# Kernel optimization log

Hardware: AMD Instinct MI355X
Metric: run time of the kernel (lower is better)

Reference implementation:

```python
import jax, jax.numpy as jnp
import numpy as np

N_NODES = 100000
N_EDGES = 3200000
IN_DIM = 128
HIDDEN = 128
N_GRAPHS = 64


def setup_inputs() -> dict:
    key = jax.random.key(0)
    ks = jax.random.split(key, 16)
    feat = jax.random.normal(ks[0], (N_NODES, IN_DIM), dtype=jnp.float32)
    src = jax.random.randint(ks[1], (N_EDGES,), 0, N_NODES, dtype=jnp.int32)
    dst = jax.random.randint(ks[2], (N_EDGES,), 0, N_NODES, dtype=jnp.int32)
    graph_ids = jnp.sort(jax.random.randint(ks[3], (N_NODES,), 0, N_GRAPHS, dtype=jnp.int32))
    # GraphConv weights (in_feats, out_feats) + bias, DGL default glorot-ish scale
    def lin(k, fi, fo):
        s = 1.0 / np.sqrt(fi)
        kw, kb = jax.random.split(k)
        W = jax.random.uniform(kw, (fi, fo), jnp.float32, -s, s)
        b = jax.random.uniform(kb, (fo,), jnp.float32, -s, s)
        return W, b
    W1, b1 = lin(ks[4], IN_DIM, HIDDEN)
    W2, b2 = lin(ks[5], HIDDEN, HIDDEN)
    # MLPReadout(128, 1, L=3): 128->64->32->16->1
    Wm0, bm0 = lin(ks[6], 128, 64)
    Wm1, bm1 = lin(ks[7], 64, 32)
    Wm2, bm2 = lin(ks[8], 32, 16)
    Wm3, bm3 = lin(ks[9], 16, 1)
    return dict(feat=feat, src=src, dst=dst, graph_ids=graph_ids, num_graphs=N_GRAPHS,
                W1=W1, b1=b1, W2=W2, b2=b2,
                Wm0=Wm0, bm0=bm0, Wm1=Wm1, bm1=bm1, Wm2=Wm2, bm2=bm2, Wm3=Wm3, bm3=bm3)


def reference(feat, src, dst, graph_ids, num_graphs,
              W1, b1, W2, b2,
              Wm0, bm0, Wm1, bm1, Wm2, bm2, Wm3, bm3):
    N = feat.shape[0]
    ones_e = jnp.ones(src.shape[0], dtype=feat.dtype)
    # DGL GraphConv norm='both': D_out^{-1/2} on src side, D_in^{-1/2} on dst side,
    # degrees clamped to >=1 (allow_zero_in_degree=True)
    deg_out = jnp.clip(jax.ops.segment_sum(ones_e, src, num_segments=N), 1.0)
    deg_in = jnp.clip(jax.ops.segment_sum(ones_e, dst, num_segments=N), 1.0)
    norm_src = jax.lax.rsqrt(deg_out)[:, None]  # [N,1]
    norm_dst = jax.lax.rsqrt(deg_in)[:, None]

    def gconv(h, W, b):
        h = h * norm_src
        agg = jax.ops.segment_sum(h[src], dst, num_segments=N)  # SpMM: [N,d]
        return agg * norm_dst @ W + b

    h = jax.nn.relu(gconv(feat, W1, b1))
    h = jax.nn.relu(gconv(h, W2, b2))

    # dgl.mean_nodes: per-graph mean over nodes
    counts = jnp.clip(jax.ops.segment_sum(jnp.ones(N, dtype=h.dtype), graph_ids, num_segments=num_graphs), 1.0)
    hg = jax.ops.segment_sum(h, graph_ids, num_segments=num_graphs) / counts[:, None]  # [G, hidden]

    # MLPReadout
    y = jax.nn.relu(hg @ Wm0 + bm0)
    y = jax.nn.relu(y @ Wm1 + bm1)
    y = jax.nn.relu(y @ Wm2 + bm2)
    return y @ Wm3 + bm3  # [G, 1]
```

## Files before the change

kernel.cpp:

```cpp
#include <hip/hip_runtime.h>
#include <hip/hip_fp16.h>

#define N_NODES 100000
#define N_EDGES 3200000
#define DIM 128
#define NG 64
#define GS_CHUNKS 16

#define KSH 9
#define BKT 512
#define NBKT ((N_NODES + BKT - 1) / BKT)
#define CHUNK 16384
#define NBLK ((N_EDGES + CHUNK - 1) / CHUNK)

using f16x8 = __attribute__((ext_vector_type(8))) _Float16;
using f32x4 = __attribute__((ext_vector_type(4))) float;

__global__ __launch_bounds__(256) void k_hist1(const int* __restrict__ src, const int* __restrict__ dst,
                                               int* __restrict__ histD, int* __restrict__ histS) {
    __shared__ int hD[NBKT];
    __shared__ int hS[NBKT];
    int t = threadIdx.x, blk = blockIdx.x;
    for (int i = t; i < NBKT; i += 256) { hD[i] = 0; hS[i] = 0; }
    __syncthreads();
    int base = blk * CHUNK;
    for (int i = t; i < CHUNK; i += 256) {
        int e = base + i;
        if (e < N_EDGES) {
            atomicAdd(&hD[dst[e] >> KSH], 1);
            atomicAdd(&hS[src[e] >> KSH], 1);
        }
    }
    __syncthreads();
    for (int i = t; i < NBKT; i += 256) {
        histD[i * NBLK + blk] = hD[i];
        histS[i * NBLK + blk] = hS[i];
    }
}

__global__ __launch_bounds__(256) void k_rowsum(const int* __restrict__ histD,
                                                const int* __restrict__ histS,
                                                int* __restrict__ rowtot) {
    __shared__ int red[256];
    int r = blockIdx.x;
    const int* a = (r < NBKT) ? (histD + (size_t)r * NBLK) : (histS + (size_t)(r - NBKT) * NBLK);
    int t = threadIdx.x;
    int s = 0;
    for (int i = t; i < NBLK; i += 256) s += a[i];
    red[t] = s;
    __syncthreads();
    for (int off = 128; off > 0; off >>= 1) {
        if (t < off) red[t] += red[t + off];
        __syncthreads();
    }
    if (t == 0) rowtot[r] = red[0];
}

__global__ void k_basescan(int* __restrict__ rowtot) {
    __shared__ int sh[256];
    int t = threadIdx.x;
    int o0 = (t < NBKT) ? rowtot[t] : 0;
    int o1 = (t < NBKT) ? rowtot[NBKT + t] : 0;
    sh[t] = o0; __syncthreads();
    for (int off = 1; off < 256; off <<= 1) {
        int v = sh[t]; int u = (t >= off) ? sh[t - off] : 0;
        __syncthreads(); sh[t] = v + u; __syncthreads();
    }
    int e0 = sh[t] - o0;
    __syncthreads();
    sh[t] = o1; __syncthreads();
    for (int off = 1; off < 256; off <<= 1) {
        int v = sh[t]; int u = (t >= off) ? sh[t - off] : 0;
        __syncthreads(); sh[t] = v + u; __syncthreads();
    }
    int e1 = sh[t] - o1;
    if (t < NBKT) { rowtot[t] = e0; rowtot[NBKT + t] = e1; }
}

__global__ __launch_bounds__(256) void k_rowapply(int* __restrict__ histD, int* __restrict__ histS,
                                                  const int* __restrict__ rowtot) {
    __shared__ int sh[256];
    int r = blockIdx.x;
    int* a = (r < NBKT) ? (histD + (size_t)r * NBLK) : (histS + (size_t)(r - NBKT) * NBLK);
    int t = threadIdx.x;
    int v = (t < NBLK) ? a[t] : 0;
    sh[t] = v; __syncthreads();
    for (int off = 1; off < 256; off <<= 1) {
        int x = sh[t]; int u = (t >= off) ? sh[t - off] : 0;
        __syncthreads(); sh[t] = x + u; __syncthreads();
    }
    int excl = sh[t] - v + rowtot[r];
    if (t < NBLK) a[t] = excl;
}

__global__ __launch_bounds__(256) void k_scatter1(const int* __restrict__ src, const int* __restrict__ dst,
                                                  const int* __restrict__ histD, const int* __restrict__ histS,
                                                  int* __restrict__ bufD, unsigned short* __restrict__ bufS) {
    __shared__ int cD[NBKT];
    __shared__ int cS[NBKT];
    int t = threadIdx.x, blk = blockIdx.x;
    for (int i = t; i < NBKT; i += 256) {
        cD[i] = histD[i * NBLK + blk];
        cS[i] = histS[i * NBLK + blk];
    }
    __syncthreads();
    int base = blk * CHUNK;
    for (int i = t; i < CHUNK; i += 256) {
        int e = base + i;
        if (e < N_EDGES) {
            int s = src[e], d = dst[e];
            int pD = atomicAdd(&cD[d >> KSH], 1);
            bufD[pD] = ((d & (BKT - 1)) << 17) | s;
            int pS = atomicAdd(&cS[s >> KSH], 1);
            bufS[pS] = (unsigned short)(s & (BKT - 1));
        }
    }
}

__global__ __launch_bounds__(256) void k_pass2s(const unsigned short* __restrict__ bufS,
                                                const int* __restrict__ histS,
                                                float* __restrict__ norm_src) {
    __shared__ int binc[BKT];
    int b = blockIdx.x, t = threadIdx.x;
    int start = histS[b * NBLK];
    int end = (b + 1 < NBKT) ? histS[(b + 1) * NBLK] : N_EDGES;
    for (int i = t; i < BKT; i += 256) binc[i] = 0;
    __syncthreads();
    for (int i = start + t; i < end; i += 256) atomicAdd(&binc[bufS[i]], 1);
    __syncthreads();
    int nb = N_NODES - b * BKT; if (nb > BKT) nb = BKT;
    for (int j = t; j < nb; j += 256) {
        int c = binc[j]; if (c < 1) c = 1;
        norm_src[b * BKT + j] = rsqrtf((float)c);
    }
}

__global__ __launch_bounds__(256) void k_pass2(const int* __restrict__ bufD,
                                               const int* __restrict__ histD,
                                               int* __restrict__ rowptr, float* __restrict__ norm_dst,
                                               int* __restrict__ col) {
    __shared__ int binc[BKT];
    __shared__ int binoff[BKT];
    int b = blockIdx.x, t = threadIdx.x;
    int start = histD[b * NBLK];
    int end = (b + 1 < NBKT) ? histD[(b + 1) * NBLK] : N_EDGES;
    for (int i = t; i < BKT; i += 256) binc[i] = 0;
    __syncthreads();
    for (int i = start + t; i < end; i += 256) atomicAdd(&binc[bufD[i] >> 17], 1);
    __syncthreads();
    if (t < 64) {
        int base8 = t * 8;
        int loc[8]; int s8 = 0;
        #pragma unroll
        for (int k = 0; k < 8; k++) { loc[k] = s8; s8 += binc[base8 + k]; }
        int x = s8;
        #pragma unroll
        for (int off = 1; off < 64; off <<= 1) {
            int y = __shfl_up(x, off);
            if (t >= off) x += y;
        }
        int excl = x - s8;
        #pragma unroll
        for (int k = 0; k < 8; k++) binoff[base8 + k] = excl + loc[k];
    }
    __syncthreads();
    int nb = N_NODES - b * BKT; if (nb > BKT) nb = BKT;
    for (int j = t; j < nb; j += 256) {
        rowptr[b * BKT + j] = start + binoff[j];
        int c = binc[j]; if (c < 1) c = 1;
        norm_dst[b * BKT + j] = rsqrtf((float)c);
    }
    if (b == NBKT - 1 && t == 0) rowptr[N_NODES] = N_EDGES;
    __syncthreads();
    for (int i = t; i < BKT; i += 256) binc[i] = binoff[i];
    __syncthreads();
    for (int i = start + t; i < end; i += 256) {
        int v = bufD[i];
        int ld = v >> 17, s = v & 0x1FFFF;
        int p = atomicAdd(&binc[ld], 1);
        col[start + p] = s;
    }
}

__global__ __launch_bounds__(256) void k_cast8(const float* __restrict__ in,
                                               const float* __restrict__ norm_src,
                                               unsigned* __restrict__ out) {
    int i4 = blockIdx.x * 256 + threadIdx.x;
    const int TOT = N_NODES * DIM / 4;
    if (i4 >= TOT) return;
    int row = i4 >> 5;
    float sc = norm_src[row];
    float4 v = ((const float4*)in)[i4];
    unsigned w = 0;
    w = __builtin_amdgcn_cvt_pk_fp8_f32(v.x * sc, v.y * sc, w, 0);
    w = __builtin_amdgcn_cvt_pk_fp8_f32(v.z * sc, v.w * sc, w, 1);
    out[i4] = w;
}

#define ACC8(r) do {                                                                  \
    auto p0 = __builtin_amdgcn_cvt_pk_f32_fp8((r).x, 0); a0 += p0[0]; a1 += p0[1];    \
    auto p1 = __builtin_amdgcn_cvt_pk_f32_fp8((r).x, 1); a2 += p1[0]; a3 += p1[1];    \
    auto p2 = __builtin_amdgcn_cvt_pk_f32_fp8((r).y, 0); a4 += p2[0]; a5 += p2[1];    \
    auto p3 = __builtin_amdgcn_cvt_pk_f32_fp8((r).y, 1); a6 += p3[0]; a7 += p3[1];    \
    auto p4 = __builtin_amdgcn_cvt_pk_f32_fp8((r).z, 0); a8 += p4[0]; a9 += p4[1];    \
    auto p5 = __builtin_amdgcn_cvt_pk_f32_fp8((r).z, 1); a10 += p5[0]; a11 += p5[1];  \
    auto p6 = __builtin_amdgcn_cvt_pk_f32_fp8((r).w, 0); a12 += p6[0]; a13 += p6[1];  \
    auto p7 = __builtin_amdgcn_cvt_pk_f32_fp8((r).w, 1); a14 += p7[0]; a15 += p7[1];  \
} while (0)

#define RED3(v) { v += __shfl_xor(v, 8); v += __shfl_xor(v, 16); v += __shfl_xor(v, 32); }

__global__ __launch_bounds__(256) void k_spmm8(const unsigned char* __restrict__ in,
                       const int* __restrict__ rowptr, const int* __restrict__ col,
                       const float* __restrict__ norm_dst, __half2* __restrict__ out) {
    int wave = (blockIdx.x * 256 + threadIdx.x) >> 6;
    int lane = threadIdx.x & 63;
    if (wave >= N_NODES) return;
    int jb = rowptr[wave], je = rowptr[wave + 1];
    int rg = lane >> 3, l8 = lane & 7;
    float a0 = 0.f, a1 = 0.f, a2 = 0.f, a3 = 0.f, a4 = 0.f, a5 = 0.f, a6 = 0.f, a7 = 0.f;
    float a8 = 0.f, a9 = 0.f, a10 = 0.f, a11 = 0.f, a12 = 0.f, a13 = 0.f, a14 = 0.f, a15 = 0.f;
    int j = jb;
    for (; j + 16 <= je; j += 16) {
        int sa = col[j + rg];
        int sb = col[j + 8 + rg];
        uint4 ra = *(const uint4*)&in[(size_t)sa * 128 + l8 * 16];
        uint4 rb = *(const uint4*)&in[(size_t)sb * 128 + l8 * 16];
        ACC8(ra);
        ACC8(rb);
    }
    if (j + 8 <= je) {
        int sa = col[j + rg];
        uint4 ra = *(const uint4*)&in[(size_t)sa * 128 + l8 * 16];
        ACC8(ra);
        j += 8;
    }
    int rem = je - j;
    if (rg < rem) {
        int sa = col[j + rg];
        uint4 ra = *(const uint4*)&in[(size_t)sa * 128 + l8 * 16];
        ACC8(ra);
    }
    RED3(a0) RED3(a1) RED3(a2) RED3(a3) RED3(a4) RED3(a5) RED3(a6) RED3(a7)
    RED3(a8) RED3(a9) RED3(a10) RED3(a11) RED3(a12) RED3(a13) RED3(a14) RED3(a15)
    if (rg == 0) {
        float nd = norm_dst[wave];
        __half2 h0 = __floats2half2_rn(a0 * nd, a1 * nd);
        __half2 h1 = __floats2half2_rn(a2 * nd, a3 * nd);
        __half2 h2 = __floats2half2_rn(a4 * nd, a5 * nd);
        __half2 h3 = __floats2half2_rn(a6 * nd, a7 * nd);
        __half2 h4 = __floats2half2_rn(a8 * nd, a9 * nd);
        __half2 h5 = __floats2half2_rn(a10 * nd, a11 * nd);
        __half2 h6 = __floats2half2_rn(a12 * nd, a13 * nd);
        __half2 h7 = __floats2half2_rn(a14 * nd, a15 * nd);
        uint4 o0, o1;
        o0.x = *(unsigned*)&h0; o0.y = *(unsigned*)&h1;
        o0.z = *(unsigned*)&h2; o0.w = *(unsigned*)&h3;
        o1.x = *(unsigned*)&h4; o1.y = *(unsigned*)&h5;
        o1.z = *(unsigned*)&h6; o1.w = *(unsigned*)&h7;
        *(uint4*)&out[(size_t)wave * 64 + l8 * 8] = o0;
        *(uint4*)&out[(size_t)wave * 64 + l8 * 8 + 4] = o1;
    }
}

template <bool SCALE, bool OUT8>
__global__ __launch_bounds__(256) void k_gemm_mfma(const __half* __restrict__ A,
        const float* __restrict__ W, const float* __restrict__ bias,
        const float* __restrict__ rowscale, void* __restrict__ outp) {
    __shared__ _Float16 lds[128 * 136];
    int tid = threadIdx.x;
    for (int idx = tid * 4; idx < DIM * DIM; idx += 256 * 4) {
        int k = idx >> 7, n = idx & 127;
        float4 w = *(const float4*)&W[idx];
        lds[(n + 0) * 136 + k] = (_Float16)w.x;
        lds[(n + 1) * 136 + k] = (_Float16)w.y;
        lds[(n + 2) * 136 + k] = (_Float16)w.z;
        lds[(n + 3) * 136 + k] = (_Float16)w.w;
    }
    __syncthreads();
    int wv = tid >> 6, lane = tid & 63;
    int rbase = blockIdx.x * 64 + wv * 16;
    int l15 = lane & 15, kg = lane >> 4;
    int arow = rbase + l15; if (arow >= N_NODES) arow = N_NODES - 1;
    const _Float16* Af = (const _Float16*)A + (size_t)arow * DIM + kg * 8;
    f16x8 a0 = *(const f16x8*)(Af + 0);
    f16x8 a1 = *(const f16x8*)(Af + 32);
    f16x8 a2 = *(const f16x8*)(Af + 64);
    f16x8 a3 = *(const f16x8*)(Af + 96);
    f32x4 acc[8];
    #pragma unroll
    for (int nt = 0; nt < 8; nt++) acc[nt] = (f32x4){0.f, 0.f, 0.f, 0.f};
    #pragma unroll
    for (int nt = 0; nt < 8; nt++) {
        const _Float16* bb = &lds[(nt * 16 + l15) * 136 + kg * 8];
        f16x8 b0 = *(const f16x8*)(bb + 0);
        f16x8 b1 = *(const f16x8*)(bb + 32);
        f16x8 b2 = *(const f16x8*)(bb + 64);
        f16x8 b3 = *(const f16x8*)(bb + 96);
        acc[nt] = __builtin_amdgcn_mfma_f32_16x16x32_f16(a0, b0, acc[nt], 0, 0, 0);
        acc[nt] = __builtin_amdgcn_mfma_f32_16x16x32_f16(a1, b1, acc[nt], 0, 0, 0);
        acc[nt] = __builtin_amdgcn_mfma_f32_16x16x32_f16(a2, b2, acc[nt], 0, 0, 0);
        acc[nt] = __builtin_amdgcn_mfma_f32_16x16x32_f16(a3, b3, acc[nt], 0, 0, 0);
    }
    __syncthreads();
    float bsc[4];
    #pragma unroll
    for (int r = 0; r < 4; r++) {
        if (SCALE) {
            int row = rbase + kg * 4 + r; if (row >= N_NODES) row = N_NODES - 1;
            bsc[r] = rowscale[row];
        } else bsc[r] = 1.f;
    }
    #pragma unroll
    for (int nt = 0; nt < 8; nt++) {
        float bv = bias[nt * 16 + l15];
        #pragma unroll
        for (int r = 0; r < 4; r++) {
            float v = fmaxf(acc[nt][r] + bv, 0.f) * bsc[r];
            lds[(size_t)(wv * 16 + kg * 4 + r) * 136 + nt * 16 + l15] = (_Float16)v;
        }
    }
    __syncthreads();
    #pragma unroll
    for (int t = 0; t < 4; t++) {
        int lrow = wv * 16 + t * 4 + kg;
        int grow = rbase + t * 4 + kg;
        f16x8 v = *(const f16x8*)&lds[(size_t)lrow * 136 + l15 * 8];
        if (grow < N_NODES) {
            if (OUT8) {
                unsigned w0 = 0, w1 = 0;
                w0 = __builtin_amdgcn_cvt_pk_fp8_f32((float)v[0], (float)v[1], w0, 0);
                w0 = __builtin_amdgcn_cvt_pk_fp8_f32((float)v[2], (float)v[3], w0, 1);
                w1 = __builtin_amdgcn_cvt_pk_fp8_f32((float)v[4], (float)v[5], w1, 0);
                w1 = __builtin_amdgcn_cvt_pk_fp8_f32((float)v[6], (float)v[7], w1, 1);
                uint2 o; o.x = w0; o.y = w1;
                *(uint2*)&((unsigned char*)outp)[(size_t)grow * 128 + l15 * 8] = o;
            } else {
                *(f16x8*)&((_Float16*)outp)[(size_t)grow * DIM + l15 * 8] = v;
            }
        }
    }
}

__global__ void k_bounds(const int* __restrict__ gids, int* __restrict__ gstart,
                         int* __restrict__ gend) {
    int g = threadIdx.x;
    if (g >= NG) return;
    int lo = 0, hi = N_NODES;
    while (lo < hi) { int mid = (lo + hi) >> 1; if (gids[mid] < g) lo = mid + 1; else hi = mid; }
    int s = lo;
    lo = 0; hi = N_NODES;
    while (lo < hi) { int mid = (lo + hi) >> 1; if (gids[mid] <= g) lo = mid + 1; else hi = mid; }
    gstart[g] = s;
    gend[g] = lo;
}

__global__ __launch_bounds__(256) void k_graphsum_part(const __half2* __restrict__ h,
                           const int* __restrict__ gstart, const int* __restrict__ gend,
                           float* __restrict__ partial) {
    __shared__ float redx[256];
    __shared__ float redy[256];
    int g = blockIdx.x;
    int c = blockIdx.y;
    int p = threadIdx.x & 63;
    int r = threadIdx.x >> 6;
    int s = gstart[g], e = gend[g];
    int clen = (e - s + GS_CHUNKS - 1) / GS_CHUNKS;
    int b0 = s + c * clen;
    int b1 = b0 + clen; if (b1 > e) b1 = e;
    float ax = 0.f, ay = 0.f;
    for (int nd = b0 + r; nd < b1; nd += 4) {
        float2 f = __half22float2(h[(size_t)nd * 64 + p]);
        ax += f.x; ay += f.y;
    }
    redx[threadIdx.x] = ax; redy[threadIdx.x] = ay;
    __syncthreads();
    if (threadIdx.x < 64) {
        float sx = redx[threadIdx.x] + redx[threadIdx.x + 64] + redx[threadIdx.x + 128] + redx[threadIdx.x + 192];
        float sy = redy[threadIdx.x] + redy[threadIdx.x + 64] + redy[threadIdx.x + 128] + redy[threadIdx.x + 192];
        float* pp = &partial[((size_t)g * GS_CHUNKS + c) * DIM];
        pp[2 * threadIdx.x] = sx;
        pp[2 * threadIdx.x + 1] = sy;
    }
}

__global__ void k_graphsum_combine(const float* __restrict__ partial,
                                   const int* __restrict__ gstart, const int* __restrict__ gend,
                                   float* __restrict__ hg) {
    int g = blockIdx.x;
    int f = threadIdx.x;
    float acc = 0.f;
    #pragma unroll
    for (int c = 0; c < GS_CHUNKS; c++)
        acc += partial[((size_t)g * GS_CHUNKS + c) * DIM + f];
    int cntv = gend[g] - gstart[g]; if (cntv < 1) cntv = 1;
    hg[g * DIM + f] = acc / (float)cntv;
}

__global__ void k_mlp(const float* __restrict__ hg,
                      const float* __restrict__ Wm0, const float* __restrict__ bm0,
                      const float* __restrict__ Wm1, const float* __restrict__ bm1,
                      const float* __restrict__ Wm2, const float* __restrict__ bm2,
                      const float* __restrict__ Wm3, const float* __restrict__ bm3,
                      float* __restrict__ out) {
    __shared__ float hb[DIM];
    __shared__ float l0[64];
    __shared__ float l1[32];
    __shared__ float l2[16];
    int g = blockIdx.x;
    int t = threadIdx.x;
    hb[t] = hg[g * DIM + t];
    hb[t + 64] = hg[g * DIM + t + 64];
    __syncthreads();
    {
        float acc = bm0[t];
        for (int k = 0; k < 128; k++) acc += hb[k] * Wm0[k * 64 + t];
        l0[t] = fmaxf(acc, 0.f);
    }
    __syncthreads();
    if (t < 32) {
        float acc = bm1[t];
        for (int k = 0; k < 64; k++) acc += l0[k] * Wm1[k * 32 + t];
        l1[t] = fmaxf(acc, 0.f);
    }
    __syncthreads();
    if (t < 16) {
        float acc = bm2[t];
        for (int k = 0; k < 32; k++) acc += l1[k] * Wm2[k * 16 + t];
        l2[t] = fmaxf(acc, 0.f);
    }
    __syncthreads();
    if (t == 0) {
        float acc = bm3[0];
        for (int k = 0; k < 16; k++) acc += l2[k] * Wm3[k];
        out[g] = acc;
    }
}

extern "C" void kernel_launch(void* const* d_in, const int* in_sizes, int n_in,
                              void* d_out, int out_size, void* d_ws, size_t ws_size,
                              hipStream_t stream) {
    const float* feat = (const float*)d_in[0];
    const int*   src  = (const int*)d_in[1];
    const int*   dst  = (const int*)d_in[2];
    const int*   gids = (const int*)d_in[3];
    const float* W1   = (const float*)d_in[5];
    const float* b1   = (const float*)d_in[6];
    const float* W2   = (const float*)d_in[7];
    const float* b2   = (const float*)d_in[8];
    const float* Wm0  = (const float*)d_in[9];
    const float* bm0  = (const float*)d_in[10];
    const float* Wm1  = (const float*)d_in[11];
    const float* bm1  = (const float*)d_in[12];
    const float* Wm2  = (const float*)d_in[13];
    const float* bm2  = (const float*)d_in[14];
    const float* Wm3  = (const float*)d_in[15];
    const float* bm3  = (const float*)d_in[16];
    float* out = (float*)d_out;

    char* ws = (char*)d_ws;
    size_t off = 0;
    auto alloc = [&](size_t bytes) -> void* {
        void* p = ws + off;
        off += (bytes + 511) & ~(size_t)511;
        return p;
    };
    float* norm_src = (float*)alloc((size_t)N_NODES * 4);
    float* norm_dst = (float*)alloc((size_t)N_NODES * 4);
    int* rowptr   = (int*)alloc((size_t)(N_NODES + 1) * 4);
    int* histD    = (int*)alloc((size_t)NBKT * NBLK * 4);
    int* histS    = (int*)alloc((size_t)NBKT * NBLK * 4);
    int* rowtot   = (int*)alloc((size_t)(2 * NBKT) * 4);
    int* bufD     = (int*)alloc((size_t)N_EDGES * 4);
    int* colbuf   = (int*)alloc((size_t)N_EDGES * 4);
    unsigned char* feat8 = (unsigned char*)alloc((size_t)N_NODES * DIM);
    unsigned char* h8    = (unsigned char*)alloc((size_t)N_NODES * DIM);
    __half* s16   = (__half*)alloc((size_t)N_NODES * DIM * 2);
    __half* g16   = (__half*)alloc((size_t)N_NODES * DIM * 2);
    float* hg     = (float*)alloc((size_t)NG * DIM * 4);
    float* partial = (float*)alloc((size_t)NG * GS_CHUNKS * DIM * 4);
    int* gstart   = (int*)alloc((size_t)NG * 4);
    int* gend     = (int*)alloc((size_t)NG * 4);
    unsigned short* bufS = (unsigned short*)colbuf;
    int* col = colbuf;

    k_hist1<<<NBLK, 256, 0, stream>>>(src, dst, histD, histS);
    k_rowsum<<<2 * NBKT, 256, 0, stream>>>(histD, histS, rowtot);
    k_basescan<<<1, 256, 0, stream>>>(rowtot);
    k_rowapply<<<2 * NBKT, 256, 0, stream>>>(histD, histS, rowtot);
    k_scatter1<<<NBLK, 256, 0, stream>>>(src, dst, histD, histS, bufD, bufS);
    k_pass2s<<<NBKT, 256, 0, stream>>>(bufS, histS, norm_src);
    k_pass2<<<NBKT, 256, 0, stream>>>(bufD, histD, rowptr, norm_dst, col);

    k_cast8<<<(N_NODES * DIM / 4 + 255) / 256, 256, 0, stream>>>(feat, norm_src, (unsigned*)feat8);

    int sb = (N_NODES + 3) / 4;
    int gb = (N_NODES + 63) / 64;
    k_spmm8<<<sb, 256, 0, stream>>>(feat8, rowptr, col, norm_dst, (__half2*)s16);
    k_gemm_mfma<true, true><<<gb, 256, 0, stream>>>(s16, W1, b1, norm_src, h8);
    k_spmm8<<<sb, 256, 0, stream>>>(h8, rowptr, col, norm_dst, (__half2*)s16);
    k_gemm_mfma<false, false><<<gb, 256, 0, stream>>>(s16, W2, b2, nullptr, g16);

    k_bounds<<<1, 64, 0, stream>>>(gids, gstart, gend);
    dim3 gsg(NG, GS_CHUNKS);
    k_graphsum_part<<<gsg, 256, 0, stream>>>((const __half2*)g16, gstart, gend, partial);
    k_graphsum_combine<<<NG, 128, 0, stream>>>(partial, gstart, gend, hg);
    k_mlp<<<NG, 64, 0, stream>>>(hg, Wm0, bm0, Wm1, bm1, Wm2, bm2, Wm3, bm3, out);
}
```

Measured before the change: 375.1 us.

## Remap SpMM to eight lanes per node and fuse small scan and readout kernels

```diff
diff --git a/kernel.cpp b/kernel.cpp
--- a/kernel.cpp
+++ b/kernel.cpp
@@ -17,7 +17,8 @@
 using f32x4 = __attribute__((ext_vector_type(4))) float;
 
 __global__ __launch_bounds__(256) void k_hist1(const int* __restrict__ src, const int* __restrict__ dst,
-                                               int* __restrict__ histD, int* __restrict__ histS) {
+                                               int* __restrict__ histD, int* __restrict__ histS,
+                                               int* __restrict__ rowtot) {
     __shared__ int hD[NBKT];
     __shared__ int hS[NBKT];
     int t = threadIdx.x, blk = blockIdx.x;
@@ -35,62 +36,34 @@
     for (int i = t; i < NBKT; i += 256) {
         histD[i * NBLK + blk] = hD[i];
         histS[i * NBLK + blk] = hS[i];
-    }
-}
-
-__global__ __launch_bounds__(256) void k_rowsum(const int* __restrict__ histD,
-                                                const int* __restrict__ histS,
-                                                int* __restrict__ rowtot) {
+        atomicAdd(&rowtot[i], hD[i]);
+        atomicAdd(&rowtot[NBKT + i], hS[i]);
+    }
+}
+
+__global__ __launch_bounds__(256) void k_rowapply(int* __restrict__ histD, int* __restrict__ histS,
+                                                  const int* __restrict__ rowtot) {
+    __shared__ int sh[256];
     __shared__ int red[256];
     int r = blockIdx.x;
-    const int* a = (r < NBKT) ? (histD + (size_t)r * NBLK) : (histS + (size_t)(r - NBKT) * NBLK);
+    int half = (r < NBKT) ? 0 : 1;
+    int pos = half ? (r - NBKT) : r;
+    int* a = half ? (histS + (size_t)pos * NBLK) : (histD + (size_t)pos * NBLK);
     int t = threadIdx.x;
-    int s = 0;
-    for (int i = t; i < NBLK; i += 256) s += a[i];
-    red[t] = s;
+    red[t] = (t < pos) ? rowtot[half * NBKT + t] : 0;
     __syncthreads();
     for (int off = 128; off > 0; off >>= 1) {
         if (t < off) red[t] += red[t + off];
         __syncthreads();
     }
-    if (t == 0) rowtot[r] = red[0];
-}
-
-__global__ void k_basescan(int* __restrict__ rowtot) {
-    __shared__ int sh[256];
-    int t = threadIdx.x;
-    int o0 = (t < NBKT) ? rowtot[t] : 0;
-    int o1 = (t < NBKT) ? rowtot[NBKT + t] : 0;
-    sh[t] = o0; __syncthreads();
+    int basev = red[0];
+    int x = (t < NBLK) ? a[t] : 0;
+    sh[t] = x; __syncthreads();
     for (int off = 1; off < 256; off <<= 1) {
-        int v = sh[t]; int u = (t >= off) ? sh[t - off] : 0;
-        __syncthreads(); sh[t] = v + u; __syncthreads();
-    }
-    int e0 = sh[t] - o0;
-    __syncthreads();
-    sh[t] = o1; __syncthreads();
-    for (int off = 1; off < 256; off <<= 1) {
-        int v = sh[t]; int u = (t >= off) ? sh[t - off] : 0;
-        __syncthreads(); sh[t] = v + u; __syncthreads();
-    }
-    int e1 = sh[t] - o1;
-    if (t < NBKT) { rowtot[t] = e0; rowtot[NBKT + t] = e1; }
-}
-
-__global__ __launch_bounds__(256) void k_rowapply(int* __restrict__ histD, int* __restrict__ histS,
-                                                  const int* __restrict__ rowtot) {
-    __shared__ int sh[256];
-    int r = blockIdx.x;
-    int* a = (r < NBKT) ? (histD + (size_t)r * NBLK) : (histS + (size_t)(r - NBKT) * NBLK);
-    int t = threadIdx.x;
-    int v = (t < NBLK) ? a[t] : 0;
-    sh[t] = v; __syncthreads();
-    for (int off = 1; off < 256; off <<= 1) {
-        int x = sh[t]; int u = (t >= off) ? sh[t - off] : 0;
-        __syncthreads(); sh[t] = x + u; __syncthreads();
-    }
-    int excl = sh[t] - v + rowtot[r];
-    if (t < NBLK) a[t] = excl;
+        int y = sh[t]; int u = (t >= off) ? sh[t - off] : 0;
+        __syncthreads(); sh[t] = y + u; __syncthreads();
+    }
+    if (t < NBLK) a[t] = sh[t] - x + basev;
 }
 
 __global__ __launch_bounds__(256) void k_scatter1(const int* __restrict__ src, const int* __restrict__ dst,
@@ -208,59 +181,46 @@
     auto p7 = __builtin_amdgcn_cvt_pk_f32_fp8((r).w, 1); a14 += p7[0]; a15 += p7[1];  \
 } while (0)
 
-#define RED3(v) { v += __shfl_xor(v, 8); v += __shfl_xor(v, 16); v += __shfl_xor(v, 32); }
-
 __global__ __launch_bounds__(256) void k_spmm8(const unsigned char* __restrict__ in,
                        const int* __restrict__ rowptr, const int* __restrict__ col,
                        const float* __restrict__ norm_dst, __half2* __restrict__ out) {
-    int wave = (blockIdx.x * 256 + threadIdx.x) >> 6;
+    int wid = (blockIdx.x * 256 + threadIdx.x) >> 6;
     int lane = threadIdx.x & 63;
-    if (wave >= N_NODES) return;
-    int jb = rowptr[wave], je = rowptr[wave + 1];
     int rg = lane >> 3, l8 = lane & 7;
+    int node = wid * 8 + rg;
+    if (node >= N_NODES) return;
+    int jb = rowptr[node], je = rowptr[node + 1];
     float a0 = 0.f, a1 = 0.f, a2 = 0.f, a3 = 0.f, a4 = 0.f, a5 = 0.f, a6 = 0.f, a7 = 0.f;
     float a8 = 0.f, a9 = 0.f, a10 = 0.f, a11 = 0.f, a12 = 0.f, a13 = 0.f, a14 = 0.f, a15 = 0.f;
     int j = jb;
-    for (; j + 16 <= je; j += 16) {
-        int sa = col[j + rg];
-        int sb = col[j + 8 + rg];
-        uint4 ra = *(const uint4*)&in[(size_t)sa * 128 + l8 * 16];
-        uint4 rb = *(const uint4*)&in[(size_t)sb * 128 + l8 * 16];
-        ACC8(ra);
-        ACC8(rb);
-    }
-    if (j + 8 <= je) {
-        int sa = col[j + rg];
-        uint4 ra = *(const uint4*)&in[(size_t)sa * 128 + l8 * 16];
-        ACC8(ra);
-        j += 8;
-    }
-    int rem = je - j;
-    if (rg < rem) {
-        int sa = col[j + rg];
-        uint4 ra = *(const uint4*)&in[(size_t)sa * 128 + l8 * 16];
-        ACC8(ra);
-    }
-    RED3(a0) RED3(a1) RED3(a2) RED3(a3) RED3(a4) RED3(a5) RED3(a6) RED3(a7)
-    RED3(a8) RED3(a9) RED3(a10) RED3(a11) RED3(a12) RED3(a13) RED3(a14) RED3(a15)
-    if (rg == 0) {
-        float nd = norm_dst[wave];
-        __half2 h0 = __floats2half2_rn(a0 * nd, a1 * nd);
-        __half2 h1 = __floats2half2_rn(a2 * nd, a3 * nd);
-        __half2 h2 = __floats2half2_rn(a4 * nd, a5 * nd);
-        __half2 h3 = __floats2half2_rn(a6 * nd, a7 * nd);
-        __half2 h4 = __floats2half2_rn(a8 * nd, a9 * nd);
-        __half2 h5 = __floats2half2_rn(a10 * nd, a11 * nd);
-        __half2 h6 = __floats2half2_rn(a12 * nd, a13 * nd);
-        __half2 h7 = __floats2half2_rn(a14 * nd, a15 * nd);
-        uint4 o0, o1;
-        o0.x = *(unsigned*)&h0; o0.y = *(unsigned*)&h1;
-        o0.z = *(unsigned*)&h2; o0.w = *(unsigned*)&h3;
-        o1.x = *(unsigned*)&h4; o1.y = *(unsigned*)&h5;
-        o1.z = *(unsigned*)&h6; o1.w = *(unsigned*)&h7;
-        *(uint4*)&out[(size_t)wave * 64 + l8 * 8] = o0;
-        *(uint4*)&out[(size_t)wave * 64 + l8 * 8 + 4] = o1;
-    }
+    for (; j + 2 <= je; j += 2) {
+        int s0 = col[j], s1 = col[j + 1];
+        uint4 r0 = *(const uint4*)&in[(size_t)s0 * 128 + l8 * 16];
+        uint4 r1 = *(const uint4*)&in[(size_t)s1 * 128 + l8 * 16];
+        ACC8(r0);
+        ACC8(r1);
+    }
+    if (j < je) {
+        int s0 = col[j];
+        uint4 r0 = *(const uint4*)&in[(size_t)s0 * 128 + l8 * 16];
+        ACC8(r0);
+    }
+    float nd = norm_dst[node];
+    __half2 h0 = __floats2half2_rn(a0 * nd, a1 * nd);
+    __half2 h1 = __floats2half2_rn(a2 * nd, a3 * nd);
+    __half2 h2 = __floats2half2_rn(a4 * nd, a5 * nd);
+    __half2 h3 = __floats2half2_rn(a6 * nd, a7 * nd);
+    __half2 h4 = __floats2half2_rn(a8 * nd, a9 * nd);
+    __half2 h5 = __floats2half2_rn(a10 * nd, a11 * nd);
+    __half2 h6 = __floats2half2_rn(a12 * nd, a13 * nd);
+    __half2 h7 = __floats2half2_rn(a14 * nd, a15 * nd);
+    uint4 o0, o1;
+    o0.x = *(unsigned*)&h0; o0.y = *(unsigned*)&h1;
+    o0.z = *(unsigned*)&h2; o0.w = *(unsigned*)&h3;
+    o1.x = *(unsigned*)&h4; o1.y = *(unsigned*)&h5;
+    o1.z = *(unsigned*)&h6; o1.w = *(unsigned*)&h7;
+    *(uint4*)&out[(size_t)node * 64 + l8 * 8] = o0;
+    *(uint4*)&out[(size_t)node * 64 + l8 * 8 + 4] = o1;
 }
 
 template <bool SCALE, bool OUT8>
@@ -342,29 +302,25 @@
     }
 }
 
-__global__ void k_bounds(const int* __restrict__ gids, int* __restrict__ gstart,
-                         int* __restrict__ gend) {
-    int g = threadIdx.x;
-    if (g >= NG) return;
-    int lo = 0, hi = N_NODES;
-    while (lo < hi) { int mid = (lo + hi) >> 1; if (gids[mid] < g) lo = mid + 1; else hi = mid; }
-    int s = lo;
-    lo = 0; hi = N_NODES;
-    while (lo < hi) { int mid = (lo + hi) >> 1; if (gids[mid] <= g) lo = mid + 1; else hi = mid; }
-    gstart[g] = s;
-    gend[g] = lo;
-}
-
 __global__ __launch_bounds__(256) void k_graphsum_part(const __half2* __restrict__ h,
-                           const int* __restrict__ gstart, const int* __restrict__ gend,
-                           float* __restrict__ partial) {
+                           const int* __restrict__ gids, float* __restrict__ partial) {
     __shared__ float redx[256];
     __shared__ float redy[256];
+    __shared__ int sb[2];
     int g = blockIdx.x;
     int c = blockIdx.y;
+    if (threadIdx.x == 0) {
+        int lo = 0, hi = N_NODES;
+        while (lo < hi) { int mid = (lo + hi) >> 1; if (gids[mid] < g) lo = mid + 1; else hi = mid; }
+        sb[0] = lo;
+        lo = 0; hi = N_NODES;
+        while (lo < hi) { int mid = (lo + hi) >> 1; if (gids[mid] <= g) lo = mid + 1; else hi = mid; }
+        sb[1] = lo;
+    }
+    __syncthreads();
+    int s = sb[0], e = sb[1];
     int p = threadIdx.x & 63;
     int r = threadIdx.x >> 6;
-    int s = gstart[g], e = gend[g];
     int clen = (e - s + GS_CHUNKS - 1) / GS_CHUNKS;
     int b0 = s + c * clen;
     int b1 = b0 + clen; if (b1 > e) b1 = e;
@@ -384,20 +340,8 @@
     }
 }
 
-__global__ void k_graphsum_combine(const float* __restrict__ partial,
-                                   const int* __restrict__ gstart, const int* __restrict__ gend,
-                                   float* __restrict__ hg) {
-    int g = blockIdx.x;
-    int f = threadIdx.x;
-    float acc = 0.f;
-    #pragma unroll
-    for (int c = 0; c < GS_CHUNKS; c++)
-        acc += partial[((size_t)g * GS_CHUNKS + c) * DIM + f];
-    int cntv = gend[g] - gstart[g]; if (cntv < 1) cntv = 1;
-    hg[g * DIM + f] = acc / (float)cntv;
-}
-
-__global__ void k_mlp(const float* __restrict__ hg,
+__global__ __launch_bounds__(128) void k_mlp(const float* __restrict__ partial,
+                      const int* __restrict__ gids,
                       const float* __restrict__ Wm0, const float* __restrict__ bm0,
                       const float* __restrict__ Wm1, const float* __restrict__ bm1,
                       const float* __restrict__ Wm2, const float* __restrict__ bm2,
@@ -407,33 +351,47 @@
     __shared__ float l0[64];
     __shared__ float l1[32];
     __shared__ float l2[16];
+    __shared__ int scnt;
     int g = blockIdx.x;
     int t = threadIdx.x;
-    hb[t] = hg[g * DIM + t];
-    hb[t + 64] = hg[g * DIM + t + 64];
-    __syncthreads();
-    {
-        float acc = bm0[t];
-        for (int k = 0; k < 128; k++) acc += hb[k] * Wm0[k * 64 + t];
-        l0[t] = fmaxf(acc, 0.f);
+    if (t == 0) {
+        int lo = 0, hi = N_NODES;
+        while (lo < hi) { int mid = (lo + hi) >> 1; if (gids[mid] < g) lo = mid + 1; else hi = mid; }
+        int s = lo;
+        lo = 0; hi = N_NODES;
+        while (lo < hi) { int mid = (lo + hi) >> 1; if (gids[mid] <= g) lo = mid + 1; else hi = mid; }
+        int c = lo - s; if (c < 1) c = 1;
+        scnt = c;
+    }
+    __syncthreads();
+    float acc = 0.f;
+    #pragma unroll
+    for (int c = 0; c < GS_CHUNKS; c++)
+        acc += partial[((size_t)g * GS_CHUNKS + c) * DIM + t];
+    hb[t] = acc / (float)scnt;
+    __syncthreads();
+    if (t < 64) {
+        float a = bm0[t];
+        for (int k = 0; k < 128; k++) a += hb[k] * Wm0[k * 64 + t];
+        l0[t] = fmaxf(a, 0.f);
     }
     __syncthreads();
     if (t < 32) {
-        float acc = bm1[t];
-        for (int k = 0; k < 64; k++) acc += l0[k] * Wm1[k * 32 + t];
-        l1[t] = fmaxf(acc, 0.f);
+        float a = bm1[t];
+        for (int k = 0; k < 64; k++) a += l0[k] * Wm1[k * 32 + t];
+        l1[t] = fmaxf(a, 0.f);
     }
     __syncthreads();
     if (t < 16) {
-        float acc = bm2[t];
-        for (int k = 0; k < 32; k++) acc += l1[k] * Wm2[k * 16 + t];
-        l2[t] = fmaxf(acc, 0.f);
+        float a = bm2[t];
+        for (int k = 0; k < 32; k++) a += l1[k] * Wm2[k * 16 + t];
+        l2[t] = fmaxf(a, 0.f);
     }
     __syncthreads();
     if (t == 0) {
-        float acc = bm3[0];
-        for (int k = 0; k < 16; k++) acc += l2[k] * Wm3[k];
-        out[g] = acc;
+        float a = bm3[0];
+        for (int k = 0; k < 16; k++) a += l2[k] * Wm3[k];
+        out[g] = a;
     }
 }
 
@@ -477,16 +435,13 @@
     unsigned char* h8    = (unsigned char*)alloc((size_t)N_NODES * DIM);
     __half* s16   = (__half*)alloc((size_t)N_NODES * DIM * 2);
     __half* g16   = (__half*)alloc((size_t)N_NODES * DIM * 2);
-    float* hg     = (float*)alloc((size_t)NG * DIM * 4);
     float* partial = (float*)alloc((size_t)NG * GS_CHUNKS * DIM * 4);
-    int* gstart   = (int*)alloc((size_t)NG * 4);
-    int* gend     = (int*)alloc((size_t)NG * 4);
     unsigned short* bufS = (unsigned short*)colbuf;
     int* col = colbuf;
 
-    k_hist1<<<NBLK, 256, 0, stream>>>(src, dst, histD, histS);
-    k_rowsum<<<2 * NBKT, 256, 0, stream>>>(histD, histS, rowtot);
-    k_basescan<<<1, 256, 0, stream>>>(rowtot);
+    hipMemsetAsync(rowtot, 0, (size_t)(2 * NBKT) * 4, stream);
+
+    k_hist1<<<NBLK, 256, 0, stream>>>(src, dst, histD, histS, rowtot);
     k_rowapply<<<2 * NBKT, 256, 0, stream>>>(histD, histS, rowtot);
     k_scatter1<<<NBLK, 256, 0, stream>>>(src, dst, histD, histS, bufD, bufS);
     k_pass2s<<<NBKT, 256, 0, stream>>>(bufS, histS, norm_src);
@@ -494,16 +449,14 @@
 
     k_cast8<<<(N_NODES * DIM / 4 + 255) / 256, 256, 0, stream>>>(feat, norm_src, (unsigned*)feat8);
 
-    int sb = (N_NODES + 3) / 4;
+    int sb2 = (N_NODES + 31) / 32;
     int gb = (N_NODES + 63) / 64;
-    k_spmm8<<<sb, 256, 0, stream>>>(feat8, rowptr, col, norm_dst, (__half2*)s16);
+    k_spmm8<<<sb2, 256, 0, stream>>>(feat8, rowptr, col, norm_dst, (__half2*)s16);
     k_gemm_mfma<true, true><<<gb, 256, 0, stream>>>(s16, W1, b1, norm_src, h8);
-    k_spmm8<<<sb, 256, 0, stream>>>(h8, rowptr, col, norm_dst, (__half2*)s16);
+    k_spmm8<<<sb2, 256, 0, stream>>>(h8, rowptr, col, norm_dst, (__half2*)s16);
     k_gemm_mfma<false, false><<<gb, 256, 0, stream>>>(s16, W2, b2, nullptr, g16);
 
-    k_bounds<<<1, 64, 0, stream>>>(gids, gstart, gend);
     dim3 gsg(NG, GS_CHUNKS);
-    k_graphsum_part<<<gsg, 256, 0, stream>>>((const __half2*)g16, gstart, gend, partial);
-    k_graphsum_combine<<<NG, 128, 0, stream>>>(partial, gstart, gend, hg);
-    k_mlp<<<NG, 64, 0, stream>>>(hg, Wm0, bm0, Wm1, bm1, Wm2, bm2, Wm3, bm3, out);
-}
+    k_graphsum_part<<<gsg, 256, 0, stream>>>((const __half2*)g16, gids, partial);
+    k_mlp<<<NG, 128, 0, stream>>>(partial, gids, Wm0, bm0, Wm1, bm1, Wm2, bm2, Wm3, bm3, out);
+}
```

After: 369.7 us. Within noise of the previous version (-1.4%).
